# Kernel optimization log

Measured on AMD Instinct MI355X. Metric: run time of the kernel, lower is better.

## Reference

```python
import jax, jax.numpy as jnp
import numpy as np

N = 4096
IN = 64          # input_size
QD = 16          # query_vector_dim
CI = 2 * IN + 1  # 129, MLP_Param input dim


def _xavier(key, shape):
    fan_in, fan_out = shape[-2], shape[-1]
    bound = float(np.sqrt(6.0 / (fan_in + fan_out)))
    return jax.random.uniform(key, shape, jnp.float32, -bound, bound)


def setup_inputs() -> dict:
    key = jax.random.key(0)
    ks = jax.random.split(key, 10)
    return {
        "x": jax.random.normal(ks[0], (N, IN + 1), jnp.float32),
        "h": jax.random.normal(ks[1], (N, IN), jnp.float32),
        "query_vectors": jax.random.normal(ks[2], (N, QD), jnp.float32),
        "adj": jax.random.uniform(ks[3], (N, N), jnp.float32),
        "nodes_ind": jnp.arange(N, dtype=jnp.int64 if jax.config.jax_enable_x64 else jnp.int32),
        "W_r": _xavier(ks[4], (QD, CI, IN)),
        "b_r": _xavier(ks[5], (QD, IN)),
        "W_u": _xavier(ks[6], (QD, CI, IN)),
        "b_u": _xavier(ks[7], (QD, IN)),
        "W_c": _xavier(ks[8], (QD, CI, IN)),
        "b_c": _xavier(ks[9], (QD, IN)),
    }


def _mlp_param(xv, q, W, b):
    # per-node dynamic weights: [n, CI, IN]
    Wn = jnp.einsum('nd,dio->nio', q, W)
    return jnp.einsum('ni,nio->no', xv, Wn) + q @ b


def reference(x, h, query_vectors, adj, nodes_ind, W_r, b_r, W_u, b_u, W_c, b_c):
    combined = adj @ jnp.concatenate([x, h], axis=-1)          # [N, 129]
    cg = combined[nodes_ind]                                    # [M, 129]
    r = jax.nn.sigmoid(_mlp_param(cg, query_vectors, W_r, b_r))
    u = jax.nn.sigmoid(_mlp_param(cg, query_vectors, W_u, b_u))
    h2 = h.at[nodes_ind].set(r * h[nodes_ind])                  # h[nodes_ind] = r*h[nodes_ind]
    combined_new = jnp.concatenate([x, h2], axis=-1)[nodes_ind]  # no adj mixing second time
    cand = jnp.tanh(_mlp_param(combined_new, query_vectors, W_c, b_c))
    return (1.0 - u) * h2[nodes_ind] + u * cand
```

## Files before the change

kernel.cpp:

```cpp
#include <hip/hip_runtime.h>
#include <math.h>


#define NN   4096
#define XCC  65
#define HCC  64
#define QDIM 16
#define CI   129
#define CST  132
#define AKST 520
#define XVST 148
#define GSTRIDE 147456

typedef unsigned short u16;
typedef __attribute__((ext_vector_type(4))) unsigned short ushort4_t;
typedef __attribute__((ext_vector_type(8))) unsigned short ushort8_t;
typedef __attribute__((ext_vector_type(8))) short bf16x8;
typedef __attribute__((ext_vector_type(16))) float f32x16;

__device__ __forceinline__ void split2(float a, u16& hi, u16& lo) {
  unsigned u = __float_as_uint(a);
  hi = (u16)(u >> 16);
  float rec = __uint_as_float(u & 0xFFFF0000u);
  float lf = a - rec;
  unsigned v = __float_as_uint(lf);
  v += 0x7FFF + ((v >> 16) & 1);
  lo = (u16)(v >> 16);
}

__device__ __forceinline__ void gload_lds16(const void* gsrc, void* ldst) {
  __builtin_amdgcn_global_load_lds(
      (const __attribute__((address_space(1))) unsigned int*)gsrc,
      (__attribute__((address_space(3))) unsigned int*)ldst, 16, 0, 0);
}

__global__ __launch_bounds__(256) void k0_pack(const float* __restrict__ x,
                                               const float* __restrict__ h,
                                               u16* __restrict__ Bh,
                                               u16* __restrict__ Bl,
                                               const float* __restrict__ Wr,
                                               const float* __restrict__ Wu,
                                               const float* __restrict__ Wc,
                                               u16* __restrict__ Wh,
                                               u16* __restrict__ Wl) {
  __shared__ float sT[64][161];
  const int t = threadIdx.x;
  if (blockIdx.x < 64) {
    const int n0 = blockIdx.x * 64;
    for (int f = t; f < 64 * XCC; f += 256) {
      int n = f / XCC, c = f - n * XCC;
      sT[n][c] = x[(size_t)(n0 + n) * XCC + c];
    }
    for (int f = t; f < 64 * HCC; f += 256) {
      int n = f >> 6, c = f & 63;
      sT[n][XCC + c] = h[(size_t)(n0 + n) * HCC + c];
    }
    for (int f = t; f < 64 * 31; f += 256) {
      int n = f / 31, c = f - n * 31;
      sT[n][CI + c] = 0.f;
    }
    __syncthreads();
    for (int idx = t; idx < 5 * 4 * 64; idx += 256) {
      const int lane = idx & 63;
      const int ksl = (idx >> 6) & 3;
      const int ct = idx >> 8;
      const int nl = ksl * 16 + (lane >> 5) * 8;
      const int feat = ct * 32 + (lane & 31);
      ushort8_t vh, vl;
#pragma unroll
      for (int j = 0; j < 8; ++j) {
        u16 hi, lo; split2(sT[nl + j][feat], hi, lo);
        vh[j] = hi; vl[j] = lo;
      }
      const size_t off = (((size_t)ct * 256 + (blockIdx.x * 4) + ksl) * 64 + lane) * 8;
      *(ushort8_t*)(Bh + off) = vh;
      *(ushort8_t*)(Bl + off) = vl;
    }
  } else {
    int gid = (blockIdx.x - 64) * 256 + t;
    if (gid >= 3 * 16 * 2 * 9 * 64) return;
    int lane = gid & 63;
    int rest = gid >> 6;
    int kst = rest % 9; rest /= 9;
    int ct = rest & 1; rest >>= 1;
    int d = rest & 15; rest >>= 4;
    const float* W = (rest == 0) ? Wr : (rest == 1 ? Wu : Wc);
    const int o = ct * 32 + (lane & 31);
    const int i0 = kst * 16 + (lane >> 5) * 8;
    ushort8_t vh, vl;
#pragma unroll
    for (int j = 0; j < 8; ++j) {
      int i = i0 + j;
      float v = (i < CI) ? W[((size_t)d * CI + i) * 64 + o] : 0.f;
      u16 hi, lo; split2(v, hi, lo);
      vh[j] = hi; vl[j] = lo;
    }
    const size_t off = (size_t)gid * 8;
    *(ushort8_t*)(Wh + off) = vh;
    *(ushort8_t*)(Wl + off) = vl;
  }
}

template <int SPKT>
__global__ __launch_bounds__(256, 4) void k1_mfma(const float* __restrict__ adj,
                                                  const u16* __restrict__ Bh,
                                                  const u16* __restrict__ Bl,
                                                  float* __restrict__ P1) {
  constexpr int KLEN = 4096 / SPKT;
  constexpr int STEPS = KLEN / 16;
  __shared__ u16 sAh[2][2][64][8];
  __shared__ u16 sAl[2][2][64][8];
  __shared__ u16 sB[3][10][512];
  __shared__ u16 sScratch[512];
  const int t = threadIdx.x;
  const int lane = t & 63;
  const int w = t >> 6;
  const int rgrp = w & 1;
  const int cthalf = w >> 1;
  const int m0 = blockIdx.x * 64;
  const int sp = blockIdx.y;
  const int ct0 = cthalf ? 3 : 0;
  const int R = t >> 2;
  const int ksts = t & 3;
  const int srg = R >> 5, srl = R & 31;
  const int skh = ksts >> 1, sj0 = (ksts & 1) * 4;

  f32x16 a0, a1, a2;
#pragma unroll
  for (int r = 0; r < 16; ++r) { a0[r] = 0.f; a1[r] = 0.f; a2[r] = 0.f; }

  const float* aptr = adj + (size_t)(m0 + R) * NN + sp * KLEN + ksts * 4;
  float4 va, vb, vc;

#define LOADA(it, tgt) tgt = *(const float4*)(aptr + (it) * 16);

#define CONV4(src, abuf)                                                       \
  {                                                                            \
    u16 h0, h1, h2, h3, l0, l1, l2, l3;                                        \
    split2(src.x, h0, l0); split2(src.y, h1, l1);                              \
    split2(src.z, h2, l2); split2(src.w, h3, l3);                              \
    ushort4_t hv = {h0, h1, h2, h3};                                           \
    ushort4_t lv = {l0, l1, l2, l3};                                           \
    *(ushort4_t*)&sAh[abuf][srg][srl + 32 * skh][sj0] = hv;                    \
    *(ushort4_t*)&sAl[abuf][srg][srl + 32 * skh][sj0] = lv;                    \
  }

#define BDMA(it, bbuf)                                                         \
  {                                                                            \
    _Pragma("unroll")                                                          \
    for (int j = 0; j < 3; ++j) {                                              \
      const int c = w + 4 * j;                                                 \
      const int ct = (c < 10) ? (c >> 1) : 0;                                  \
      const int hl = (c < 10) ? (c & 1) : 0;                                   \
      const int ks = sp * STEPS + (it);                                        \
      const u16* src =                                                         \
          (hl ? Bl : Bh) + (((size_t)ct * 256 + ks) * 64 + lane) * 8;          \
      gload_lds16(src, (c < 10) ? &sB[bbuf][c][0] : &sScratch[0]);             \
    }                                                                          \
  }

#define BAR(N)                                                                 \
  asm volatile("s_waitcnt vmcnt(" #N ") lgkmcnt(0)" ::: "memory");             \
  __builtin_amdgcn_sched_barrier(0);                                           \
  __builtin_amdgcn_s_barrier();                                                \
  __builtin_amdgcn_sched_barrier(0);

#define COMPUTE(abuf, bbuf)                                                    \
  {                                                                            \
    bf16x8 ah = *(const bf16x8*)&sAh[abuf][rgrp][lane][0];                     \
    bf16x8 al = *(const bf16x8*)&sAl[abuf][rgrp][lane][0];                     \
    const int cb = ct0 * 2;                                                    \
    bf16x8 b0h = *(const bf16x8*)&sB[bbuf][cb + 0][lane * 8];                  \
    bf16x8 b0l = *(const bf16x8*)&sB[bbuf][cb + 1][lane * 8];                  \
    bf16x8 b1h = *(const bf16x8*)&sB[bbuf][cb + 2][lane * 8];                  \
    bf16x8 b1l = *(const bf16x8*)&sB[bbuf][cb + 3][lane * 8];                  \
    a0 = __builtin_amdgcn_mfma_f32_32x32x16_bf16(ah, b0h, a0, 0, 0, 0);        \
    a1 = __builtin_amdgcn_mfma_f32_32x32x16_bf16(ah, b1h, a1, 0, 0, 0);        \
    a0 = __builtin_amdgcn_mfma_f32_32x32x16_bf16(al, b0h, a0, 0, 0, 0);        \
    a1 = __builtin_amdgcn_mfma_f32_32x32x16_bf16(al, b1h, a1, 0, 0, 0);        \
    a0 = __builtin_amdgcn_mfma_f32_32x32x16_bf16(ah, b0l, a0, 0, 0, 0);        \
    a1 = __builtin_amdgcn_mfma_f32_32x32x16_bf16(ah, b1l, a1, 0, 0, 0);        \
    if (cthalf == 0) {                                                         \
      bf16x8 b2h = *(const bf16x8*)&sB[bbuf][cb + 4][lane * 8];                \
      bf16x8 b2l = *(const bf16x8*)&sB[bbuf][cb + 5][lane * 8];                \
      a2 = __builtin_amdgcn_mfma_f32_32x32x16_bf16(ah, b2h, a2, 0, 0, 0);      \
      a2 = __builtin_amdgcn_mfma_f32_32x32x16_bf16(al, b2h, a2, 0, 0, 0);      \
      a2 = __builtin_amdgcn_mfma_f32_32x32x16_bf16(ah, b2l, a2, 0, 0, 0);      \
    }                                                                          \
  }

  LOADA(0, va);
  BDMA(0, 0);
  LOADA(1, vb);
  BDMA(1, 1);
  LOADA(2, vc);
  CONV4(va, 0);
  BAR(5)
#pragma unroll
  for (int it = 0; it < STEPS; ++it) {
    const int abuf = it & 1;
    const int bbuf = it % 3;
    if (it < STEPS - 2) BDMA(it + 2, (it + 2) % 3);
    if (it <= STEPS - 4) {
      if ((it % 3) == 0) { LOADA(it + 3, va); }
      else if ((it % 3) == 1) { LOADA(it + 3, vb); }
      else { LOADA(it + 3, vc); }
    }
    COMPUTE(abuf, bbuf);
    if (it < STEPS - 1) {
      if (((it + 1) % 3) == 0) { CONV4(va, abuf ^ 1); }
      else if (((it + 1) % 3) == 1) { CONV4(vb, abuf ^ 1); }
      else { CONV4(vc, abuf ^ 1); }
    }
    if (it <= STEPS - 4) { BAR(5) }
    else if (it == STEPS - 3) { BAR(4) }
    else if (it == STEPS - 2) { BAR(0) }
  }
#undef LOADA
#undef CONV4
#undef BDMA
#undef BAR
#undef COMPUTE
  float* outp = P1 + (size_t)sp * NN * CST;
  const int colb = lane & 31;
  const int rbase = m0 + rgrp * 32 + 4 * (lane >> 5);
  {
    const int colg = ct0 * 32 + colb;
#pragma unroll
    for (int r = 0; r < 16; ++r)
      outp[(size_t)(rbase + (r & 3) + 8 * (r >> 2)) * CST + colg] = a0[r];
  }
  {
    const int colg = (ct0 + 1) * 32 + colb;
    if (colg < CST) {
#pragma unroll
      for (int r = 0; r < 16; ++r)
        outp[(size_t)(rbase + (r & 3) + 8 * (r >> 2)) * CST + colg] = a1[r];
    }
  }
  if (cthalf == 0) {
    const int colg = 64 + colb;
#pragma unroll
    for (int r = 0; r < 16; ++r)
      outp[(size_t)(rbase + (r & 3) + 8 * (r >> 2)) * CST + colg] = a2[r];
  }
}


#define PACKA()                                                                \
  for (int s = t; s < 9 * 64; s += 512) {                                      \
    int kst = s >> 6, l = s & 63;                                              \
    int row = l & 31, k0i = kst * 16 + (l >> 5) * 8;                           \
    ushort8_t vh, vl;                                                          \
    _Pragma("unroll")                                                          \
    for (int j = 0; j < 8; ++j) {                                              \
      u16 hi, lo; split2(sXV[row][k0i + j], hi, lo);                           \
      vh[j] = hi; vl[j] = lo;                                                  \
    }                                                                          \
    *(ushort8_t*)&sAh[kst * AKST + l * 8] = vh;                                \
    *(ushort8_t*)&sAl[kst * AKST + l * 8] = vl;                                \
  }

#define XCHG(src, dst)                                                         \
  {                                                                            \
    _Pragma("unroll")                                                          \
    for (int r = 0; r < 16; ++r) sX[dh][r][lane] = src[r];                     \
    __syncthreads();                                                           \
    _Pragma("unroll")                                                          \
    for (int i = 0; i < 2; ++i) {                                              \
      const int rr = dh * 2 + i;                                               \
      float s = 0.f;                                                           \
      _Pragma("unroll")                                                        \
      for (int wv = 0; wv < 8; ++wv) s += sX[wv][rr][lane];                    \
      dst[i] = s;                                                              \
    }                                                                          \
  }

template <int SPKT>
__global__ __launch_bounds__(512) void k23_fused(
    const float* __restrict__ P1, const float* __restrict__ x,
    const float* __restrict__ h, const float* __restrict__ q,
    const u16* __restrict__ Wh, const u16* __restrict__ Wl,
    const float* __restrict__ br, const float* __restrict__ bu,
    const float* __restrict__ bc, float* __restrict__ out) {
  __shared__ float sXV[32][XVST];
  __shared__ u16 sAh[9 * AKST], sAl[9 * AKST];
  __shared__ float sQ[32][16];
  __shared__ float sX[8][16][64];
  const int t = threadIdx.x;
  const int n0 = blockIdx.x * 32;
  const int cto = blockIdx.y;
  for (int f = t; f < 32 * 33; f += 512) {
    int n = f / 33, c4 = f - n * 33;
    const float* p = P1 + (size_t)(n0 + n) * CST + c4 * 4;
    float sx = 0.f, sy = 0.f, sz = 0.f, sw = 0.f;
#pragma unroll
    for (int sp = 0; sp < SPKT; ++sp) {
      float4 v = *(const float4*)(p + (size_t)sp * NN * CST);
      sx += v.x; sy += v.y; sz += v.z; sw += v.w;
    }
    sXV[n][c4 * 4 + 0] = sx; sXV[n][c4 * 4 + 1] = sy;
    sXV[n][c4 * 4 + 2] = sz; sXV[n][c4 * 4 + 3] = sw;
  }
  for (int f = t; f < 32 * 3; f += 512) {
    float4 z = {0, 0, 0, 0};
    *(float4*)&sXV[f / 3][132 + (f % 3) * 4] = z;
  }
  sQ[t >> 4][t & 15] = q[(size_t)(n0 + (t >> 4)) * QDIM + (t & 15)];
  __syncthreads();
  PACKA();
  __syncthreads();
  for (int f = t; f < 32 * 65; f += 512) {
    int n = f / 65, i = f - n * 65;
    sXV[n][i] = x[(size_t)(n0 + n) * XCC + i];
  }
  const int lane = t & 63, dh = t >> 6;

  f32x16 aR0, aR1, aU;
#pragma unroll
  for (int r = 0; r < 16; ++r) { aR0[r] = 0.f; aR1[r] = 0.f; aU[r] = 0.f; }
#pragma unroll
  for (int dd = 0; dd < 2; ++dd) {
    const int d = dh * 2 + dd;
    const size_t bR0 = (((size_t)d * 2 + 0) * 9 * 64 + lane) * 8;
    const size_t bR1 = (((size_t)d * 2 + 1) * 9 * 64 + lane) * 8;
    const size_t bU  = (((size_t)d * 2 + cto) * 9 * 64 + lane) * 8 + GSTRIDE;
    f32x16 t0, t1, t2;
#pragma unroll
    for (int r = 0; r < 16; ++r) { t0[r] = 0.f; t1[r] = 0.f; t2[r] = 0.f; }
#pragma unroll
    for (int kst = 0; kst < 9; ++kst) {
      bf16x8 ah = *(const bf16x8*)&sAh[kst * AKST + lane * 8];
      bf16x8 al = *(const bf16x8*)&sAl[kst * AKST + lane * 8];
      bf16x8 b0h = *(const bf16x8*)(Wh + bR0 + kst * 512);
      bf16x8 b0l = *(const bf16x8*)(Wl + bR0 + kst * 512);
      bf16x8 b1h = *(const bf16x8*)(Wh + bR1 + kst * 512);
      bf16x8 b1l = *(const bf16x8*)(Wl + bR1 + kst * 512);
      bf16x8 buh = *(const bf16x8*)(Wh + bU + kst * 512);
      bf16x8 bul = *(const bf16x8*)(Wl + bU + kst * 512);
      t0 = __builtin_amdgcn_mfma_f32_32x32x16_bf16(ah, b0h, t0, 0, 0, 0);
      t1 = __builtin_amdgcn_mfma_f32_32x32x16_bf16(ah, b1h, t1, 0, 0, 0);
      t2 = __builtin_amdgcn_mfma_f32_32x32x16_bf16(ah, buh, t2, 0, 0, 0);
      t0 = __builtin_amdgcn_mfma_f32_32x32x16_bf16(al, b0h, t0, 0, 0, 0);
      t1 = __builtin_amdgcn_mfma_f32_32x32x16_bf16(al, b1h, t1, 0, 0, 0);
      t2 = __builtin_amdgcn_mfma_f32_32x32x16_bf16(al, buh, t2, 0, 0, 0);
      t0 = __builtin_amdgcn_mfma_f32_32x32x16_bf16(ah, b0l, t0, 0, 0, 0);
      t1 = __builtin_amdgcn_mfma_f32_32x32x16_bf16(ah, b1l, t1, 0, 0, 0);
      t2 = __builtin_amdgcn_mfma_f32_32x32x16_bf16(ah, bul, t2, 0, 0, 0);
    }
#pragma unroll
    for (int r = 0; r < 16; ++r) {
      int node = (r & 3) + 8 * (r >> 2) + 4 * (lane >> 5);
      float qd = sQ[node][d];
      aR0[r] += qd * t0[r]; aR1[r] += qd * t1[r]; aU[r] += qd * t2[r];
    }
  }

  float r0p[2], r1p[2], up[2];
  XCHG(aR0, r0p);
  __syncthreads();
  XCHG(aR1, r1p);
  __syncthreads();
  XCHG(aU, up);

  auto add_bias = [&](const float* bias, int node, int col, float pre) {
#pragma unroll
    for (int d = 0; d < 16; ++d) pre += sQ[node][d] * bias[(size_t)d * 64 + col];
    return pre;
  };

  const int col0 = lane & 31, col1 = 32 + col0, colu = cto * 32 + col0;
  float uval[2], h2own[2];
#pragma unroll
  for (int i = 0; i < 2; ++i) {
    const int rr = dh * 2 + i;
    const int node = (rr & 3) + 8 * (rr >> 2) + 4 * (lane >> 5);
    float pr0 = add_bias(br, node, col0, r0p[i]);
    float pr1 = add_bias(br, node, col1, r1p[i]);
    float pu  = add_bias(bu, node, colu, up[i]);
    float rg0 = 1.f / (1.f + expf(-pr0));
    float rg1 = 1.f / (1.f + expf(-pr1));
    uval[i] = 1.f / (1.f + expf(-pu));
    float h2a = rg0 * h[(size_t)(n0 + node) * HCC + col0];
    float h2b = rg1 * h[(size_t)(n0 + node) * HCC + col1];
    sXV[node][XCC + col0] = h2a;
    sXV[node][XCC + col1] = h2b;
    h2own[i] = cto ? h2b : h2a;
  }
  __syncthreads();
  PACKA();
  __syncthreads();

  {
    const u16* gh = Wh + (size_t)2 * GSTRIDE;
    const u16* gl = Wl + (size_t)2 * GSTRIDE;
    f32x16 acc;
#pragma unroll
    for (int r = 0; r < 16; ++r) acc[r] = 0.f;
#pragma unroll
    for (int dd = 0; dd < 2; ++dd) {
      const int d = dh * 2 + dd;
      const size_t bb = (((size_t)d * 2 + cto) * 9 * 64 + lane) * 8;
      f32x16 t0, t1, t2;
#pragma unroll
      for (int r = 0; r < 16; ++r) { t0[r] = 0.f; t1[r] = 0.f; t2[r] = 0.f; }
#pragma unroll
      for (int kst = 0; kst < 9; ++kst) {
        bf16x8 ah = *(const bf16x8*)&sAh[kst * AKST + lane * 8];
        bf16x8 al = *(const bf16x8*)&sAl[kst * AKST + lane * 8];
        bf16x8 bh = *(const bf16x8*)(gh + bb + kst * 512);
        bf16x8 bl = *(const bf16x8*)(gl + bb + kst * 512);
        t0 = __builtin_amdgcn_mfma_f32_32x32x16_bf16(ah, bh, t0, 0, 0, 0);
        t1 = __builtin_amdgcn_mfma_f32_32x32x16_bf16(al, bh, t1, 0, 0, 0);
        t2 = __builtin_amdgcn_mfma_f32_32x32x16_bf16(ah, bl, t2, 0, 0, 0);
      }
#pragma unroll
      for (int r = 0; r < 16; ++r) {
        int node = (r & 3) + 8 * (r >> 2) + 4 * (lane >> 5);
        acc[r] += sQ[node][d] * (t0[r] + t1[r] + t2[r]);
      }
    }
    float cp[2];
    XCHG(acc, cp);
#pragma unroll
    for (int i = 0; i < 2; ++i) {
      const int rr = dh * 2 + i;
      const int node = (rr & 3) + 8 * (rr >> 2) + 4 * (lane >> 5);
      float pc = add_bias(bc, node, colu, cp[i]);
      float cand = tanhf(pc);
      out[(size_t)(n0 + node) * HCC + colu] =
          (1.f - uval[i]) * h2own[i] + uval[i] * cand;
    }
  }
}

extern "C" void kernel_launch(void* const* d_in, const int* in_sizes, int n_in,
                              void* d_out, int out_size, void* d_ws, size_t ws_size,
                              hipStream_t stream) {
  const float* x   = (const float*)d_in[0];
  const float* h   = (const float*)d_in[1];
  const float* q   = (const float*)d_in[2];
  const float* adj = (const float*)d_in[3];
  const float* Wr  = (const float*)d_in[5];
  const float* br  = (const float*)d_in[6];
  const float* Wu  = (const float*)d_in[7];
  const float* bu  = (const float*)d_in[8];
  const float* Wc  = (const float*)d_in[9];
  const float* bc  = (const float*)d_in[10];
  float* out = (float*)d_out;

  const size_t NEED16 = (size_t)16 * NN * CST * 4 + 2162688 + 10485760 + 1769472;
  const int spk = (ws_size >= NEED16) ? 16 : 8;

  char* ws = (char*)d_ws;
  const size_t OFF_P1 = 0;
  const size_t OFF_BP = OFF_P1 + (size_t)spk * NN * CST * 4;
  const size_t OFF_WH = OFF_BP + (size_t)2 * 5 * 256 * 64 * 8 * 2;
  const size_t OFF_WL = OFF_WH + (size_t)3 * GSTRIDE * 2;
  float* P1 = (float*)(ws + OFF_P1);
  u16*   Bh = (u16*)(ws + OFF_BP);
  u16*   Bl = (u16*)(ws + OFF_BP + (size_t)5 * 256 * 64 * 8 * 2);
  u16*   Wh = (u16*)(ws + OFF_WH);
  u16*   Wl = (u16*)(ws + OFF_WL);

  hipLaunchKernelGGL(k0_pack, dim3(280), dim3(256), 0, stream,
                     x, h, Bh, Bl, Wr, Wu, Wc, Wh, Wl);
  if (spk == 16) {
    hipLaunchKernelGGL(k1_mfma<16>, dim3(64, 16), dim3(256), 0, stream,
                       adj, Bh, Bl, P1);
    hipLaunchKernelGGL(k23_fused<16>, dim3(128, 2), dim3(512), 0, stream,
                       P1, x, h, q, Wh, Wl, br, bu, bc, out);
  } else {
    hipLaunchKernelGGL(k1_mfma<8>, dim3(64, 8), dim3(256), 0, stream,
                       adj, Bh, Bl, P1);
    hipLaunchKernelGGL(k23_fused<8>, dim3(128, 2), dim3(512), 0, stream,
                       P1, x, h, q, Wh, Wl, br, bu, bc, out);
  }
}
```

Before: 69.61 us.

## Double fused gate kernel block size so each wave handles one query dim

The fused gate/candidate kernel now launches 1024 threads per block, so each of 16 waves owns a single query dimension instead of looping over two. The per-wave partial results are reduced across 16 waves in shared memory, and each thread finalises one output element instead of two. The aim is more in-flight waves to hide weight-load latency in the MFMA loops, at the cost of a larger shared reduction buffer, more threads contending at barriers, and possibly lower occupancy per CU.

```diff
diff --git a/kernel.cpp b/kernel.cpp
--- a/kernel.cpp
+++ b/kernel.cpp
@@ -246,9 +246,8 @@
   }
 }
 
-
 #define PACKA()                                                                \
-  for (int s = t; s < 9 * 64; s += 512) {                                      \
+  for (int s = t; s < 9 * 64; s += 1024) {                                     \
     int kst = s >> 6, l = s & 63;                                              \
     int row = l & 31, k0i = kst * 16 + (l >> 5) * 8;                           \
     ushort8_t vh, vl;                                                          \
@@ -261,23 +260,8 @@
     *(ushort8_t*)&sAl[kst * AKST + l * 8] = vl;                                \
   }
 
-#define XCHG(src, dst)                                                         \
-  {                                                                            \
-    _Pragma("unroll")                                                          \
-    for (int r = 0; r < 16; ++r) sX[dh][r][lane] = src[r];                     \
-    __syncthreads();                                                           \
-    _Pragma("unroll")                                                          \
-    for (int i = 0; i < 2; ++i) {                                              \
-      const int rr = dh * 2 + i;                                               \
-      float s = 0.f;                                                           \
-      _Pragma("unroll")                                                        \
-      for (int wv = 0; wv < 8; ++wv) s += sX[wv][rr][lane];                    \
-      dst[i] = s;                                                              \
-    }                                                                          \
-  }
-
 template <int SPKT>
-__global__ __launch_bounds__(512) void k23_fused(
+__global__ __launch_bounds__(1024) void k23_fused(
     const float* __restrict__ P1, const float* __restrict__ x,
     const float* __restrict__ h, const float* __restrict__ q,
     const u16* __restrict__ Wh, const u16* __restrict__ Wl,
@@ -286,11 +270,11 @@
   __shared__ float sXV[32][XVST];
   __shared__ u16 sAh[9 * AKST], sAl[9 * AKST];
   __shared__ float sQ[32][16];
-  __shared__ float sX[8][16][64];
+  __shared__ float sX[16][16][64];
   const int t = threadIdx.x;
   const int n0 = blockIdx.x * 32;
   const int cto = blockIdx.y;
-  for (int f = t; f < 32 * 33; f += 512) {
+  for (int f = t; f < 32 * 33; f += 1024) {
     int n = f / 33, c4 = f - n * 33;
     const float* p = P1 + (size_t)(n0 + n) * CST + c4 * 4;
     float sx = 0.f, sy = 0.f, sz = 0.f, sw = 0.f;
@@ -302,32 +286,27 @@
     sXV[n][c4 * 4 + 0] = sx; sXV[n][c4 * 4 + 1] = sy;
     sXV[n][c4 * 4 + 2] = sz; sXV[n][c4 * 4 + 3] = sw;
   }
-  for (int f = t; f < 32 * 3; f += 512) {
+  for (int f = t; f < 32 * 3; f += 1024) {
     float4 z = {0, 0, 0, 0};
     *(float4*)&sXV[f / 3][132 + (f % 3) * 4] = z;
   }
-  sQ[t >> 4][t & 15] = q[(size_t)(n0 + (t >> 4)) * QDIM + (t & 15)];
+  if (t < 512) sQ[t >> 4][t & 15] = q[(size_t)(n0 + (t >> 4)) * QDIM + (t & 15)];
   __syncthreads();
   PACKA();
   __syncthreads();
-  for (int f = t; f < 32 * 65; f += 512) {
+  for (int f = t; f < 32 * 65; f += 1024) {
     int n = f / 65, i = f - n * 65;
     sXV[n][i] = x[(size_t)(n0 + n) * XCC + i];
   }
   const int lane = t & 63, dh = t >> 6;
 
-  f32x16 aR0, aR1, aU;
-#pragma unroll
-  for (int r = 0; r < 16; ++r) { aR0[r] = 0.f; aR1[r] = 0.f; aU[r] = 0.f; }
-#pragma unroll
-  for (int dd = 0; dd < 2; ++dd) {
-    const int d = dh * 2 + dd;
-    const size_t bR0 = (((size_t)d * 2 + 0) * 9 * 64 + lane) * 8;
-    const size_t bR1 = (((size_t)d * 2 + 1) * 9 * 64 + lane) * 8;
-    const size_t bU  = (((size_t)d * 2 + cto) * 9 * 64 + lane) * 8 + GSTRIDE;
-    f32x16 t0, t1, t2;
-#pragma unroll
-    for (int r = 0; r < 16; ++r) { t0[r] = 0.f; t1[r] = 0.f; t2[r] = 0.f; }
+  f32x16 t0, t1, t2;
+#pragma unroll
+  for (int r = 0; r < 16; ++r) { t0[r] = 0.f; t1[r] = 0.f; t2[r] = 0.f; }
+  {
+    const size_t bR0 = (((size_t)dh * 2 + 0) * 576 + lane) * 8;
+    const size_t bR1 = (((size_t)dh * 2 + 1) * 576 + lane) * 8;
+    const size_t bU  = (((size_t)dh * 2 + cto) * 576 + lane) * 8 + GSTRIDE;
 #pragma unroll
     for (int kst = 0; kst < 9; ++kst) {
       bf16x8 ah = *(const bf16x8*)&sAh[kst * AKST + lane * 8];
@@ -348,89 +327,103 @@
       t1 = __builtin_amdgcn_mfma_f32_32x32x16_bf16(ah, b1l, t1, 0, 0, 0);
       t2 = __builtin_amdgcn_mfma_f32_32x32x16_bf16(ah, bul, t2, 0, 0, 0);
     }
-#pragma unroll
-    for (int r = 0; r < 16; ++r) {
-      int node = (r & 3) + 8 * (r >> 2) + 4 * (lane >> 5);
-      float qd = sQ[node][d];
-      aR0[r] += qd * t0[r]; aR1[r] += qd * t1[r]; aU[r] += qd * t2[r];
-    }
-  }
-
-  float r0p[2], r1p[2], up[2];
-  XCHG(aR0, r0p);
-  __syncthreads();
-  XCHG(aR1, r1p);
-  __syncthreads();
-  XCHG(aU, up);
-
-  auto add_bias = [&](const float* bias, int node, int col, float pre) {
-#pragma unroll
-    for (int d = 0; d < 16; ++d) pre += sQ[node][d] * bias[(size_t)d * 64 + col];
-    return pre;
-  };
+  }
+
+  float r0p, r1p, up;
+#pragma unroll
+  for (int r = 0; r < 16; ++r) {
+    int nd = (r & 3) + 8 * (r >> 2) + 4 * (lane >> 5);
+    sX[dh][r][lane] = sQ[nd][dh] * t0[r];
+  }
+  __syncthreads();
+  {
+    float s = 0.f;
+#pragma unroll
+    for (int wv = 0; wv < 16; ++wv) s += sX[wv][dh][lane];
+    r0p = s;
+  }
+  __syncthreads();
+#pragma unroll
+  for (int r = 0; r < 16; ++r) {
+    int nd = (r & 3) + 8 * (r >> 2) + 4 * (lane >> 5);
+    sX[dh][r][lane] = sQ[nd][dh] * t1[r];
+  }
+  __syncthreads();
+  {
+    float s = 0.f;
+#pragma unroll
+    for (int wv = 0; wv < 16; ++wv) s += sX[wv][dh][lane];
+    r1p = s;
+  }
+  __syncthreads();
+#pragma unroll
+  for (int r = 0; r < 16; ++r) {
+    int nd = (r & 3) + 8 * (r >> 2) + 4 * (lane >> 5);
+    sX[dh][r][lane] = sQ[nd][dh] * t2[r];
+  }
+  __syncthreads();
+  {
+    float s = 0.f;
+#pragma unroll
+    for (int wv = 0; wv < 16; ++wv) s += sX[wv][dh][lane];
+    up = s;
+  }
 
   const int col0 = lane & 31, col1 = 32 + col0, colu = cto * 32 + col0;
-  float uval[2], h2own[2];
-#pragma unroll
-  for (int i = 0; i < 2; ++i) {
-    const int rr = dh * 2 + i;
-    const int node = (rr & 3) + 8 * (rr >> 2) + 4 * (lane >> 5);
-    float pr0 = add_bias(br, node, col0, r0p[i]);
-    float pr1 = add_bias(br, node, col1, r1p[i]);
-    float pu  = add_bias(bu, node, colu, up[i]);
-    float rg0 = 1.f / (1.f + expf(-pr0));
-    float rg1 = 1.f / (1.f + expf(-pr1));
-    uval[i] = 1.f / (1.f + expf(-pu));
-    float h2a = rg0 * h[(size_t)(n0 + node) * HCC + col0];
-    float h2b = rg1 * h[(size_t)(n0 + node) * HCC + col1];
-    sXV[node][XCC + col0] = h2a;
-    sXV[node][XCC + col1] = h2b;
-    h2own[i] = cto ? h2b : h2a;
-  }
+  const int mynode = (dh & 3) + 8 * (dh >> 2) + 4 * (lane >> 5);
+  float pr0 = r0p, pr1 = r1p, pu = up;
+#pragma unroll
+  for (int d2 = 0; d2 < 16; ++d2) {
+    float qd = sQ[mynode][d2];
+    pr0 += qd * br[(size_t)d2 * 64 + col0];
+    pr1 += qd * br[(size_t)d2 * 64 + col1];
+    pu  += qd * bu[(size_t)d2 * 64 + colu];
+  }
+  float rg0 = 1.f / (1.f + expf(-pr0));
+  float rg1 = 1.f / (1.f + expf(-pr1));
+  float uval = 1.f / (1.f + expf(-pu));
+  float h2a = rg0 * h[(size_t)(n0 + mynode) * HCC + col0];
+  float h2b = rg1 * h[(size_t)(n0 + mynode) * HCC + col1];
+  sXV[mynode][XCC + col0] = h2a;
+  sXV[mynode][XCC + col1] = h2b;
+  float h2own = cto ? h2b : h2a;
   __syncthreads();
   PACKA();
   __syncthreads();
 
+  f32x16 c0, c1, c2;
+#pragma unroll
+  for (int r = 0; r < 16; ++r) { c0[r] = 0.f; c1[r] = 0.f; c2[r] = 0.f; }
   {
     const u16* gh = Wh + (size_t)2 * GSTRIDE;
     const u16* gl = Wl + (size_t)2 * GSTRIDE;
-    f32x16 acc;
-#pragma unroll
-    for (int r = 0; r < 16; ++r) acc[r] = 0.f;
-#pragma unroll
-    for (int dd = 0; dd < 2; ++dd) {
-      const int d = dh * 2 + dd;
-      const size_t bb = (((size_t)d * 2 + cto) * 9 * 64 + lane) * 8;
-      f32x16 t0, t1, t2;
-#pragma unroll
-      for (int r = 0; r < 16; ++r) { t0[r] = 0.f; t1[r] = 0.f; t2[r] = 0.f; }
-#pragma unroll
-      for (int kst = 0; kst < 9; ++kst) {
-        bf16x8 ah = *(const bf16x8*)&sAh[kst * AKST + lane * 8];
-        bf16x8 al = *(const bf16x8*)&sAl[kst * AKST + lane * 8];
-        bf16x8 bh = *(const bf16x8*)(gh + bb + kst * 512);
-        bf16x8 bl = *(const bf16x8*)(gl + bb + kst * 512);
-        t0 = __builtin_amdgcn_mfma_f32_32x32x16_bf16(ah, bh, t0, 0, 0, 0);
-        t1 = __builtin_amdgcn_mfma_f32_32x32x16_bf16(al, bh, t1, 0, 0, 0);
-        t2 = __builtin_amdgcn_mfma_f32_32x32x16_bf16(ah, bl, t2, 0, 0, 0);
-      }
-#pragma unroll
-      for (int r = 0; r < 16; ++r) {
-        int node = (r & 3) + 8 * (r >> 2) + 4 * (lane >> 5);
-        acc[r] += sQ[node][d] * (t0[r] + t1[r] + t2[r]);
-      }
-    }
-    float cp[2];
-    XCHG(acc, cp);
-#pragma unroll
-    for (int i = 0; i < 2; ++i) {
-      const int rr = dh * 2 + i;
-      const int node = (rr & 3) + 8 * (rr >> 2) + 4 * (lane >> 5);
-      float pc = add_bias(bc, node, colu, cp[i]);
-      float cand = tanhf(pc);
-      out[(size_t)(n0 + node) * HCC + colu] =
-          (1.f - uval[i]) * h2own[i] + uval[i] * cand;
-    }
+    const size_t bb = (((size_t)dh * 2 + cto) * 576 + lane) * 8;
+#pragma unroll
+    for (int kst = 0; kst < 9; ++kst) {
+      bf16x8 ah = *(const bf16x8*)&sAh[kst * AKST + lane * 8];
+      bf16x8 al = *(const bf16x8*)&sAl[kst * AKST + lane * 8];
+      bf16x8 bh = *(const bf16x8*)(gh + bb + kst * 512);
+      bf16x8 bl = *(const bf16x8*)(gl + bb + kst * 512);
+      c0 = __builtin_amdgcn_mfma_f32_32x32x16_bf16(ah, bh, c0, 0, 0, 0);
+      c1 = __builtin_amdgcn_mfma_f32_32x32x16_bf16(al, bh, c1, 0, 0, 0);
+      c2 = __builtin_amdgcn_mfma_f32_32x32x16_bf16(ah, bl, c2, 0, 0, 0);
+    }
+  }
+#pragma unroll
+  for (int r = 0; r < 16; ++r) {
+    int nd = (r & 3) + 8 * (r >> 2) + 4 * (lane >> 5);
+    sX[dh][r][lane] = sQ[nd][dh] * (c0[r] + c1[r] + c2[r]);
+  }
+  __syncthreads();
+  {
+    float s = 0.f;
+#pragma unroll
+    for (int wv = 0; wv < 16; ++wv) s += sX[wv][dh][lane];
+#pragma unroll
+    for (int d2 = 0; d2 < 16; ++d2) s += sQ[mynode][d2] * bc[(size_t)d2 * 64 + colu];
+    float cand = tanhf(s);
+    out[(size_t)(n0 + mynode) * HCC + colu] =
+        (1.f - uval) * h2own + uval * cand;
   }
 }
 
@@ -468,12 +461,12 @@
   if (spk == 16) {
     hipLaunchKernelGGL(k1_mfma<16>, dim3(64, 16), dim3(256), 0, stream,
                        adj, Bh, Bl, P1);
-    hipLaunchKernelGGL(k23_fused<16>, dim3(128, 2), dim3(512), 0, stream,
+    hipLaunchKernelGGL(k23_fused<16>, dim3(128, 2), dim3(1024), 0, stream,
                        P1, x, h, q, Wh, Wl, br, bu, bc, out);
   } else {
     hipLaunchKernelGGL(k1_mfma<8>, dim3(64, 8), dim3(256), 0, stream,
                        adj, Bh, Bl, P1);
-    hipLaunchKernelGGL(k23_fused<8>, dim3(128, 2), dim3(512), 0, stream,
+    hipLaunchKernelGGL(k23_fused<8>, dim3(128, 2), dim3(1024), 0, stream,
                        P1, x, h, q, Wh, Wl, br, bu, bc, out);
   }
 }
```

Measured after the change: 69.80 us. About the same (+0.3%).
